# Performance work log

Hardware: AMD Instinct MI355X
Metric: run time of the kernel (lower is better)

The kernel has to match this reference:

```python
import jax, jax.numpy as jnp
import numpy as np

N_ATOMS, N_BONDS, B = 3072, 12288, 64
D, H, L = 256, 8, 4
AF, BF = 74, 12
HD = D // H
EPS = 1e-5


def layer_norm(x, g, b):
    m = jnp.mean(x, -1, keepdims=True)
    v = jnp.mean((x - m) ** 2, -1, keepdims=True)
    return (x - m) / jnp.sqrt(v + EPS) * g + b


def mha(x, in_w, in_b, out_w, out_b, mask=None):
    # torch nn.MultiheadAttention with packed in_proj, batch of 1 sequence
    n = x.shape[0]
    qkv = x @ in_w.T + in_b                      # [n, 3D]
    q, k, v = jnp.split(qkv, 3, axis=-1)
    q = q.reshape(n, H, HD)
    k = k.reshape(n, H, HD)
    v = v.reshape(n, H, HD)
    scores = jnp.einsum('qhd,khd->hqk', q, k) / jnp.asarray(np.sqrt(HD), x.dtype)
    if mask is not None:
        scores = jnp.where(mask[None], scores, jnp.asarray(-1e9, x.dtype))
    att = jax.nn.softmax(scores, axis=-1)
    out = jnp.einsum('hqk,khd->qhd', att, v).reshape(n, D)
    return out @ out_w.T + out_b


def setup_inputs() -> dict:
    key = jax.random.key(0)
    ks = jax.random.split(key, 12)
    s = 0.05
    return {
        'atom_features': jax.random.normal(ks[0], (N_ATOMS, AF), jnp.float32),
        'bond_features': jax.random.normal(ks[1], (N_BONDS, BF), jnp.float32),
        'edge_indices': jax.random.randint(ks[2], (2, N_BONDS), 0, N_ATOMS),
        'batch_idx': jnp.sort(jax.random.randint(ks[3], (N_ATOMS,), 0, B)),
        'atom_w': jax.random.normal(ks[4], (D, AF), jnp.float32) * s,
        'atom_b': jnp.zeros((D,), jnp.float32),
        'bond_w': jax.random.normal(ks[5], (D, BF), jnp.float32) * s,
        'bond_b': jnp.zeros((D,), jnp.float32),
        'conv_w': jax.random.normal(ks[6], (L, D, 2 * D), jnp.float32) * s,
        'conv_b': jnp.zeros((L, D), jnp.float32),
        'attn_in_w': jax.random.normal(ks[7], (L, 3 * D, D), jnp.float32) * s,
        'attn_in_b': jnp.zeros((L, 3 * D), jnp.float32),
        'attn_out_w': jax.random.normal(ks[8], (L, D, D), jnp.float32) * s,
        'attn_out_b': jnp.zeros((L, D), jnp.float32),
        'ln_g': jnp.ones((L, D), jnp.float32),
        'ln_b': jnp.zeros((L, D), jnp.float32),
        'gattn_in_w': jax.random.normal(ks[9], (3 * D, D), jnp.float32) * s,
        'gattn_in_b': jnp.zeros((3 * D,), jnp.float32),
        'gattn_out_w': jax.random.normal(ks[10], (D, D), jnp.float32) * s,
        'gattn_out_b': jnp.zeros((D,), jnp.float32),
        'gn_g': jnp.ones((D,), jnp.float32),
        'gn_b': jnp.zeros((D,), jnp.float32),
    }


def reference(atom_features, bond_features, edge_indices, batch_idx,
              atom_w, atom_b, bond_w, bond_b, conv_w, conv_b,
              attn_in_w, attn_in_b, attn_out_w, attn_out_b, ln_g, ln_b,
              gattn_in_w, gattn_in_b, gattn_out_w, gattn_out_b, gn_g, gn_b):
    atom_h = atom_features @ atom_w.T + atom_b       # [N, D]
    bond_h = bond_features @ bond_w.T + bond_b       # [E, D]
    src, tgt = edge_indices[0], edge_indices[1]
    for i in range(L):
        # gather -> concat -> linear -> relu -> scatter-add
        messages = jnp.concatenate([atom_h[src] + bond_h, atom_h[tgt]], axis=-1)
        messages = jax.nn.relu(messages @ conv_w[i].T + conv_b[i])
        aggregated = jnp.zeros_like(atom_h).at[tgt].add(messages)
        # self-attention over all atoms as a single sequence (as in source)
        attended = mha(atom_h, attn_in_w[i], attn_in_b[i], attn_out_w[i], attn_out_b[i])
        atom_h = layer_norm(atom_h + aggregated + attended, ln_g[i], ln_b[i])
    # per-graph pooled attention == full attention masked to same-graph pairs
    same_graph = batch_idx[:, None] == batch_idx[None, :]
    pooled = mha(atom_h, gattn_in_w, gattn_in_b, gattn_out_w, gattn_out_b, mask=same_graph)
    pooled = layer_norm(pooled, gn_g, gn_b)
    sums = jax.ops.segment_sum(pooled, batch_idx, num_segments=B)
    counts = jax.ops.segment_sum(jnp.ones((pooled.shape[0],), pooled.dtype), batch_idx, num_segments=B)
    return sums / jnp.maximum(counts, 1.0)[:, None]   # empty graphs -> zeros, as in source
```

## Files before the change

kernel.cpp:

```cpp
#include <hip/hip_runtime.h>
#include <hip/hip_bf16.h>
#include <math.h>

#define NATOMS 3072
#define NBONDS 12288
#define NGRAPH 64
#define DIM 256
#define NH 8
#define HDIM 32
#define NLAYER 4
#define AFD 74
#define BFD 12
#define LNEPS 1e-5f
#define HSZ (NATOMS * HDIM)

typedef __attribute__((ext_vector_type(8))) short bf16x8;
typedef __attribute__((ext_vector_type(4))) short s16x4;
typedef __attribute__((ext_vector_type(4))) float f32x4;

static __device__ __forceinline__ short f2bf(float x) {
  union { float f; unsigned u; } v; v.f = x;
  unsigned r = v.u + 0x7fff + ((v.u >> 16) & 1);
  return (short)(r >> 16);
}

static __device__ __forceinline__ float4 bf4tof4(s16x4 v) {
  union { unsigned u; float f; } x0, x1, x2, x3;
  x0.u = (unsigned)(unsigned short)v[0] << 16;
  x1.u = (unsigned)(unsigned short)v[1] << 16;
  x2.u = (unsigned)(unsigned short)v[2] << 16;
  x3.u = (unsigned)(unsigned short)v[3] << 16;
  return make_float4(x0.f, x1.f, x2.f, x3.f);
}

static __device__ __forceinline__ size_t afrag(int m, int c) {
  return ((size_t)(m >> 4) * 8 + (c >> 5)) * 512 + (m & 15) * 32 + (c & 31);
}

static __device__ __forceinline__ void gemm_core(
    const short* __restrict__ arow, const short* __restrict__ wch, f32x4* acc) {
  bf16x8 Xall[8];
  #pragma unroll
  for (int kc = 0; kc < 8; ++kc) Xall[kc] = *(const bf16x8*)(arow + kc * 512);
  bf16x8 Wb[2][4];
  #pragma unroll
  for (int sub = 0; sub < 4; ++sub) Wb[0][sub] = *(const bf16x8*)(wch + sub * 512);
  #pragma unroll
  for (int kc = 0; kc < 8; ++kc) {
    const int cur = kc & 1, nxt = cur ^ 1;
    if (kc < 7) {
      #pragma unroll
      for (int sub = 0; sub < 4; ++sub)
        Wb[nxt][sub] = *(const bf16x8*)(wch + (kc + 1) * 2048 + sub * 512);
    }
    __builtin_amdgcn_sched_barrier(0);
    #pragma unroll
    for (int sub = 0; sub < 4; ++sub)
      acc[sub] = __builtin_amdgcn_mfma_f32_16x16x32_bf16(Wb[cur][sub], Xall[kc], acc[sub], 0, 0, 0);
  }
}

#define CONVW_N8 65536
#define INW_N8   98304
#define OUTW_N8  32768
#define GINW_N8  24576
#define GOUTW_N8 8192
#define REPK_TOT (CONVW_N8 + INW_N8 + OUTW_N8 + GINW_N8 + GOUTW_N8)

static __device__ __forceinline__ void repack_one(
    const float* __restrict__ W, short* __restrict__ out, int kcShift, int o8) {
  const int g = o8 & 3, lq = (o8 >> 2) & 15, sub = (o8 >> 6) & 3;
  const int chunk = o8 >> 8;
  const int kc = chunk & ((1 << kcShift) - 1);
  const int nt = chunk >> kcShift;
  const int K = 32 << kcShift;
  const int n = nt * 64 + sub * 16 + lq;
  const int c = kc * 32 + g * 8;
  const float* src = W + (size_t)n * K + c;
  bf16x8 o;
  #pragma unroll
  for (int j = 0; j < 8; ++j) o[j] = f2bf(src[j]);
  ((bf16x8*)out)[o8] = o;
}

__global__ __launch_bounds__(256) void proj_hist_kernel(
    const float* __restrict__ afeat, const float* __restrict__ aw,
    const float* __restrict__ ab, float* __restrict__ atom_h,
    short* __restrict__ atom_hb, const float* __restrict__ bfeat,
    const float* __restrict__ bw, const float* __restrict__ bb,
    short* __restrict__ bond_hb, const int* __restrict__ tgt,
    int* __restrict__ counts) {
  const int idx = blockIdx.x, t = threadIdx.x;
  if (idx < NATOMS) {
    __shared__ float x[AFD];
    if (t < AFD) x[t] = afeat[idx * AFD + t];
    __syncthreads();
    float acc = ab[t];
    const float* wr = aw + t * AFD;
    for (int k = 0; k < AFD; ++k) acc = fmaf(wr[k], x[k], acc);
    atom_h[idx * DIM + t] = acc;
    atom_hb[afrag(idx, t)] = f2bf(acc);
  } else if (idx < NATOMS + NBONDS) {
    const int e = idx - NATOMS;
    __shared__ float xb[BFD];
    if (t < BFD) xb[t] = bfeat[e * BFD + t];
    __syncthreads();
    float acc = bb[t];
    const float* wr = bw + t * BFD;
    #pragma unroll
    for (int k = 0; k < BFD; ++k) acc = fmaf(wr[k], xb[k], acc);
    bond_hb[afrag(e, t)] = f2bf(acc);
  } else {
    const int e = (idx - NATOMS - NBONDS) * 256 + t;
    if (e < NBONDS) atomicAdd(&counts[tgt[e]], 1);
  }
}

__global__ __launch_bounds__(256) void scan_kernel(
    const int* __restrict__ counts, int* __restrict__ rowptr,
    int* __restrict__ cursor) {
  __shared__ int part[256];
  const int t = threadIdx.x;
  int loc[12], s = 0;
  #pragma unroll
  for (int j = 0; j < 12; ++j) { loc[j] = counts[t * 12 + j]; s += loc[j]; }
  part[t] = s;
  __syncthreads();
  for (int o = 1; o < 256; o <<= 1) {
    const int v = (t >= o) ? part[t - o] : 0;
    __syncthreads();
    part[t] += v;
    __syncthreads();
  }
  int running = part[t] - s;
  #pragma unroll
  for (int j = 0; j < 12; ++j) {
    rowptr[t * 12 + j] = running;
    cursor[t * 12 + j] = running;
    running += loc[j];
  }
  if (t == 255) rowptr[NATOMS] = running;
}

__global__ __launch_bounds__(256) void scatter_repack_kernel(
    const int* __restrict__ tgt, int* __restrict__ cursor, int* __restrict__ elist,
    const float* __restrict__ conv_w, const float* __restrict__ in_w,
    const float* __restrict__ out_w, const float* __restrict__ gin_w,
    const float* __restrict__ gout_w, short* __restrict__ conv_wb,
    short* __restrict__ in_wb, short* __restrict__ out_wb,
    short* __restrict__ gin_wb, short* __restrict__ gout_wb) {
  const int idx = blockIdx.x;
  if (idx < 48) {
    const int e = idx * 256 + threadIdx.x;
    if (e < NBONDS) {
      const int pos = atomicAdd(&cursor[tgt[e]], 1);
      elist[pos] = e;
    }
    return;
  }
  int o8 = (idx - 48) * 256 + threadIdx.x;
  if (o8 >= REPK_TOT) return;
  if (o8 < CONVW_N8) { repack_one(conv_w, conv_wb, 4, o8); return; }
  o8 -= CONVW_N8;
  if (o8 < INW_N8) { repack_one(in_w, in_wb, 3, o8); return; }
  o8 -= INW_N8;
  if (o8 < OUTW_N8) { repack_one(out_w, out_wb, 3, o8); return; }
  o8 -= OUTW_N8;
  if (o8 < GINW_N8) { repack_one(gin_w, gin_wb, 3, o8); return; }
  o8 -= GINW_N8;
  repack_one(gout_w, gout_wb, 3, o8);
}

__global__ __launch_bounds__(256) void layer_front_kernel(
    const short* __restrict__ atom_hb, const short* __restrict__ bond_hb,
    const short* __restrict__ cw, const short* __restrict__ inw,
    const float* __restrict__ inb, short* __restrict__ B1,
    short* __restrict__ G1, short* __restrict__ G2,
    short* __restrict__ Qb, short* __restrict__ Kff, short* __restrict__ Vtf,
    float qscale) {
  const int t = threadIdx.x;
  const int w = t >> 6, l = t & 63;
  const int lq = l & 15, g = l >> 4;
  const int lof = lq * 32 + g * 8;
  const int idx = blockIdx.x;
  f32x4 acc[4] = {{0.f,0.f,0.f,0.f},{0.f,0.f,0.f,0.f},{0.f,0.f,0.f,0.f},{0.f,0.f,0.f,0.f}};

  if (idx < 768) {
    const int by = idx / 384, bx = idx % 384;
    const int mrow = bx * 32 + (w & 1) * 16 + lq;
    const int nbase = by * 128 + (w >> 1) * 64;
    gemm_core(bond_hb + (size_t)(mrow >> 4) * 8 * 512 + lof,
              cw + (size_t)(nbase >> 6) * 16 * 2048 + lof, acc);
    #pragma unroll
    for (int sub = 0; sub < 4; ++sub) {
      const int n = nbase + sub * 16 + g * 4;
      s16x4 o;
      o[0] = f2bf(acc[sub][0]); o[1] = f2bf(acc[sub][1]);
      o[2] = f2bf(acc[sub][2]); o[3] = f2bf(acc[sub][3]);
      *(s16x4*)&B1[(size_t)mrow * DIM + n] = o;
    }
  } else if (idx < 1152) {
    const int i2 = idx - 768;
    const int bx = i2 % 96, by = i2 / 96;
    const int mrow = bx * 32 + (w & 1) * 16 + lq;
    const int nbase = by * 128 + (w >> 1) * 64;
    const int half = nbase >> 8, nl = nbase & 255;
    gemm_core(atom_hb + (size_t)(mrow >> 4) * 8 * 512 + lof,
              cw + ((size_t)(nl >> 6) * 16 + half * 8) * 2048 + lof, acc);
    short* C = half ? G2 : G1;
    #pragma unroll
    for (int sub = 0; sub < 4; ++sub) {
      const int n = nl + sub * 16 + g * 4;
      s16x4 o;
      o[0] = f2bf(acc[sub][0]); o[1] = f2bf(acc[sub][1]);
      o[2] = f2bf(acc[sub][2]); o[3] = f2bf(acc[sub][3]);
      *(s16x4*)&C[(size_t)mrow * DIM + n] = o;
    }
  } else {
    const int i3 = idx - 1152;
    const int bx = i3 % 96, by = i3 / 96;
    const int mrow = bx * 32 + (w & 1) * 16 + lq;
    const int nbase = by * 128 + (w >> 1) * 64;
    gemm_core(atom_hb + (size_t)(mrow >> 4) * 8 * 512 + lof,
              inw + (size_t)(nbase >> 6) * 8 * 2048 + lof, acc);
    const int key = mrow;
    #pragma unroll
    for (int sub = 0; sub < 4; ++sub) {
      const int n = nbase + sub * 16 + g * 4;
      const float4 b4 = *(const float4*)&inb[n];
      float4 v = make_float4(acc[sub][0] + b4.x, acc[sub][1] + b4.y,
                             acc[sub][2] + b4.z, acc[sub][3] + b4.w);
      if (n < 256) {
        s16x4 o;
        o[0] = f2bf(v.x * qscale); o[1] = f2bf(v.y * qscale);
        o[2] = f2bf(v.z * qscale); o[3] = f2bf(v.w * qscale);
        *(s16x4*)&Qb[afrag(mrow, n)] = o;
      } else if (n < 512) {
        const int d = n - 256, h = d >> 5, dd = d & 31;
        const size_t base = (size_t)h * HSZ + (size_t)(key >> 6) * 2048 +
                            (size_t)((key & 63) >> 4) * 512 +
                            ((dd >> 3) * 16 + (key & 15)) * 8 + (dd & 7);
        s16x4 o;
        o[0] = f2bf(v.x); o[1] = f2bf(v.y); o[2] = f2bf(v.z); o[3] = f2bf(v.w);
        *(s16x4*)&Kff[base] = o;
      } else {
        const int d = n - 512, h = d >> 5;
        const int kt = (key & 63) >> 5, gg = (key & 31) >> 3, j = key & 7;
        const int hh = (d & 31) >> 4;
        const size_t base = (size_t)h * HSZ + (size_t)(key >> 6) * 2048 +
                            (size_t)(kt * 2 + hh) * 512 + gg * 128 + j;
        Vtf[base + (size_t)((d + 0) & 15) * 8] = f2bf(v.x);
        Vtf[base + (size_t)((d + 1) & 15) * 8] = f2bf(v.y);
        Vtf[base + (size_t)((d + 2) & 15) * 8] = f2bf(v.z);
        Vtf[base + (size_t)((d + 3) & 15) * 8] = f2bf(v.w);
      }
    }
  }
}

static __device__ __forceinline__ void attn_body_full(
    int qtile, int h, const short* __restrict__ Qb,
    const short* __restrict__ Kff, const short* __restrict__ Vtf,
    short* __restrict__ outbf) {
  __shared__ short Ps[4][2][16 * 72];
  __shared__ float Comb[3][64][18];

  const int t = threadIdx.x;
  const int wid = t >> 6;
  const int l = t & 63;
  const int lq = l & 15;
  const int g = l >> 4;
  const int qt0 = qtile * 32;

  const bf16x8 Qf0 = *(const bf16x8*)(Qb + ((size_t)(qt0 >> 4) * 8 + h) * 512 + lq * 32 + g * 8);
  const bf16x8 Qf1 = *(const bf16x8*)(Qb + ((size_t)(qt0 >> 4) * 8 + 8 + h) * 512 + lq * 32 + g * 8);

  bf16x8 OnesF;
  #pragma unroll
  for (int j = 0; j < 8; ++j) OnesF[j] = (short)0x3F80;

  const short* kh = Kff + (size_t)h * HSZ + l * 8;
  const short* vh = Vtf + (size_t)h * HSZ + l * 8;

  f32x4 accO[2][2] = {{{0.f,0.f,0.f,0.f},{0.f,0.f,0.f,0.f}},
                      {{0.f,0.f,0.f,0.f},{0.f,0.f,0.f,0.f}}};
  f32x4 accL[2] = {{0.f,0.f,0.f,0.f},{0.f,0.f,0.f,0.f}};

  const int kbeg = wid * (NATOMS / 4);
  const int kend = kbeg + NATOMS / 4;

  bf16x8 Kf[2][4];
  bf16x8 Vf[2][4];

#define LOAD_TILE(buf, kc)                                                      \
  {                                                                             \
    const size_t tb = (size_t)((kc) >> 6) * 2048;                               \
    _Pragma("unroll")                                                           \
    for (int kk = 0; kk < 4; ++kk)                                              \
      Kf[buf][kk] = *(const bf16x8*)(kh + tb + kk * 512);                       \
    _Pragma("unroll")                                                           \
    for (int ff = 0; ff < 4; ++ff)                                              \
      Vf[buf][ff] = *(const bf16x8*)(vh + tb + ff * 512);                       \
  }

  LOAD_TILE(0, kbeg);

  for (int k0 = kbeg; k0 < kend; k0 += 128) {
    #pragma unroll
    for (int ph = 0; ph < 2; ++ph) {
      const int kcur = k0 + ph * 64;
      int kn = kcur + 64;
      if (kn >= kend) kn = kbeg;
      const int pb = ph ^ 1;
      LOAD_TILE(pb, kn);
      __builtin_amdgcn_sched_barrier(0);

      #pragma unroll
      for (int qt = 0; qt < 2; ++qt) {
        const bf16x8 Qf = qt ? Qf1 : Qf0;
        short* myPs = Ps[wid][qt];
        f32x4 s[4];
        #pragma unroll
        for (int kk = 0; kk < 4; ++kk)
          s[kk] = __builtin_amdgcn_mfma_f32_16x16x32_bf16(
              Kf[ph][kk], Qf, (f32x4){0.f, 0.f, 0.f, 0.f}, 0, 0, 0);
        #pragma unroll
        for (int kk = 0; kk < 4; ++kk) {
          const float p0 = __builtin_amdgcn_exp2f(s[kk][0]);
          const float p1 = __builtin_amdgcn_exp2f(s[kk][1]);
          const float p2 = __builtin_amdgcn_exp2f(s[kk][2]);
          const float p3 = __builtin_amdgcn_exp2f(s[kk][3]);
          unsigned u0, u1;
          asm("v_cvt_pk_bf16_f32 %0, %1, %2" : "=v"(u0) : "v"(p0), "v"(p1));
          asm("v_cvt_pk_bf16_f32 %0, %1, %2" : "=v"(u1) : "v"(p2), "v"(p3));
          *(uint2*)&myPs[lq * 72 + kk * 16 + g * 4] = make_uint2(u0, u1);
        }
      }

      #pragma unroll
      for (int qt = 0; qt < 2; ++qt) {
        #pragma unroll
        for (int kt = 0; kt < 2; ++kt) {
          const bf16x8 Pf = *(const bf16x8*)&Ps[wid][qt][lq * 72 + kt * 32 + g * 8];
          #pragma unroll
          for (int hh = 0; hh < 2; ++hh)
            accO[qt][hh] = __builtin_amdgcn_mfma_f32_16x16x32_bf16(
                Vf[ph][kt * 2 + hh], Pf, accO[qt][hh], 0, 0, 0);
          accL[qt] = __builtin_amdgcn_mfma_f32_16x16x32_bf16(OnesF, Pf, accL[qt], 0, 0, 0);
        }
      }
    }
  }
#undef LOAD_TILE

  if (wid > 0) {
    #pragma unroll
    for (int qt = 0; qt < 2; ++qt) {
      Comb[wid - 1][l][qt * 9] = accL[qt][0];
      #pragma unroll
      for (int hh = 0; hh < 2; ++hh)
        #pragma unroll
        for (int r = 0; r < 4; ++r)
          Comb[wid - 1][l][qt * 9 + 1 + hh * 4 + r] = accO[qt][hh][r];
    }
  }
  __syncthreads();
  if (wid == 0) {
    #pragma unroll
    for (int qt = 0; qt < 2; ++qt) {
      float tot = accL[qt][0];
      #pragma unroll
      for (int w2 = 0; w2 < 3; ++w2) {
        tot += Comb[w2][l][qt * 9];
        #pragma unroll
        for (int hh = 0; hh < 2; ++hh)
          #pragma unroll
          for (int r = 0; r < 4; ++r)
            accO[qt][hh][r] += Comb[w2][l][qt * 9 + 1 + hh * 4 + r];
      }
      const float inv = 1.f / tot;
      const int qrow = qt0 + qt * 16 + lq;
      #pragma unroll
      for (int hh = 0; hh < 2; ++hh) {
        s16x4 o;
        #pragma unroll
        for (int r = 0; r < 4; ++r) o[r] = f2bf(accO[qt][hh][r] * inv);
        *(s16x4*)&outbf[afrag(qrow, h * HDIM + hh * 16 + g * 4)] = o;
      }
    }
  }
}

static __device__ __forceinline__ void attn_body_masked(
    int qtile, int h, const short* __restrict__ Qb,
    const short* __restrict__ Kff, const short* __restrict__ Vtf,
    const int* __restrict__ bidx, short* __restrict__ outbf) {
  __shared__ short Ps[4][2][16 * 72];
  __shared__ float Comb[3][64][18];
  __shared__ int srange[2];

  const int t = threadIdx.x;
  const int wid = t >> 6;
  const int l = t & 63;
  const int lq = l & 15;
  const int g = l >> 4;
  const int qt0 = qtile * 32;

  if (t < 2) {
    const int target = (t == 0) ? bidx[qt0] : (bidx[qt0 + 31] + 1);
    int lo = 0, hi = NATOMS;
    while (lo < hi) {
      const int mid = (lo + hi) >> 1;
      if (bidx[mid] < target) lo = mid + 1; else hi = mid;
    }
    srange[t] = lo;
  }

  const bf16x8 Qf0 = *(const bf16x8*)(Qb + ((size_t)(qt0 >> 4) * 8 + h) * 512 + lq * 32 + g * 8);
  const bf16x8 Qf1 = *(const bf16x8*)(Qb + ((size_t)(qt0 >> 4) * 8 + 8 + h) * 512 + lq * 32 + g * 8);
  const int qg0 = bidx[qt0 + lq];
  const int qg1 = bidx[qt0 + 16 + lq];

  bf16x8 OnesF;
  #pragma unroll
  for (int j = 0; j < 8; ++j) OnesF[j] = (short)0x3F80;

  const short* kh = Kff + (size_t)h * HSZ + l * 8;
  const short* vh = Vtf + (size_t)h * HSZ + l * 8;

  f32x4 accO[2][2] = {{{0.f,0.f,0.f,0.f},{0.f,0.f,0.f,0.f}},
                      {{0.f,0.f,0.f,0.f},{0.f,0.f,0.f,0.f}}};
  f32x4 accL[2] = {{0.f,0.f,0.f,0.f},{0.f,0.f,0.f,0.f}};

  __syncthreads();
  const int t0 = srange[0] >> 6;
  const int t1 = (srange[1] + 63) >> 6;

  for (int tt = t0 + wid; tt < t1; tt += 4) {
    const int kc = tt * 64;
    const size_t tb = (size_t)tt * 2048;
    bf16x8 Kf[4], Vf[4];
    int4 KBv[4];
    #pragma unroll
    for (int kk = 0; kk < 4; ++kk) Kf[kk] = *(const bf16x8*)(kh + tb + kk * 512);
    #pragma unroll
    for (int ff = 0; ff < 4; ++ff) Vf[ff] = *(const bf16x8*)(vh + tb + ff * 512);
    #pragma unroll
    for (int kk = 0; kk < 4; ++kk) KBv[kk] = *(const int4*)(bidx + kc + kk * 16 + g * 4);

    #pragma unroll
    for (int qt = 0; qt < 2; ++qt) {
      const bf16x8 Qf = qt ? Qf1 : Qf0;
      const int qg = qt ? qg1 : qg0;
      short* myPs = Ps[wid][qt];
      f32x4 s[4];
      #pragma unroll
      for (int kk = 0; kk < 4; ++kk)
        s[kk] = __builtin_amdgcn_mfma_f32_16x16x32_bf16(
            Kf[kk], Qf, (f32x4){0.f, 0.f, 0.f, 0.f}, 0, 0, 0);
      #pragma unroll
      for (int kk = 0; kk < 4; ++kk) {
        float p0 = __builtin_amdgcn_exp2f(s[kk][0]);
        float p1 = __builtin_amdgcn_exp2f(s[kk][1]);
        float p2 = __builtin_amdgcn_exp2f(s[kk][2]);
        float p3 = __builtin_amdgcn_exp2f(s[kk][3]);
        const int4 kb = KBv[kk];
        p0 = (kb.x == qg) ? p0 : 0.f;
        p1 = (kb.y == qg) ? p1 : 0.f;
        p2 = (kb.z == qg) ? p2 : 0.f;
        p3 = (kb.w == qg) ? p3 : 0.f;
        unsigned u0, u1;
        asm("v_cvt_pk_bf16_f32 %0, %1, %2" : "=v"(u0) : "v"(p0), "v"(p1));
        asm("v_cvt_pk_bf16_f32 %0, %1, %2" : "=v"(u1) : "v"(p2), "v"(p3));
        *(uint2*)&myPs[lq * 72 + kk * 16 + g * 4] = make_uint2(u0, u1);
      }
    }

    #pragma unroll
    for (int qt = 0; qt < 2; ++qt) {
      #pragma unroll
      for (int kt = 0; kt < 2; ++kt) {
        const bf16x8 Pf = *(const bf16x8*)&Ps[wid][qt][lq * 72 + kt * 32 + g * 8];
        #pragma unroll
        for (int hh = 0; hh < 2; ++hh)
          accO[qt][hh] = __builtin_amdgcn_mfma_f32_16x16x32_bf16(
              Vf[kt * 2 + hh], Pf, accO[qt][hh], 0, 0, 0);
        accL[qt] = __builtin_amdgcn_mfma_f32_16x16x32_bf16(OnesF, Pf, accL[qt], 0, 0, 0);
      }
    }
  }

  if (wid > 0) {
    #pragma unroll
    for (int qt = 0; qt < 2; ++qt) {
      Comb[wid - 1][l][qt * 9] = accL[qt][0];
      #pragma unroll
      for (int hh = 0; hh < 2; ++hh)
        #pragma unroll
        for (int r = 0; r < 4; ++r)
          Comb[wid - 1][l][qt * 9 + 1 + hh * 4 + r] = accO[qt][hh][r];
    }
  }
  __syncthreads();
  if (wid == 0) {
    #pragma unroll
    for (int qt = 0; qt < 2; ++qt) {
      float tot = accL[qt][0];
      #pragma unroll
      for (int w2 = 0; w2 < 3; ++w2) {
        tot += Comb[w2][l][qt * 9];
        #pragma unroll
        for (int hh = 0; hh < 2; ++hh)
          #pragma unroll
          for (int r = 0; r < 4; ++r)
            accO[qt][hh][r] += Comb[w2][l][qt * 9 + 1 + hh * 4 + r];
      }
      const float inv = 1.f / tot;
      const int qrow = qt0 + qt * 16 + lq;
      #pragma unroll
      for (int hh = 0; hh < 2; ++hh) {
        s16x4 o;
        #pragma unroll
        for (int r = 0; r < 4; ++r) o[r] = f2bf(accO[qt][hh][r] * inv);
        *(s16x4*)&outbf[afrag(qrow, h * HDIM + hh * 16 + g * 4)] = o;
      }
    }
  }
}

static __device__ __forceinline__ void msg_body(
    int blk, const short* __restrict__ G1, const short* __restrict__ B1,
    const short* __restrict__ G2, const float* __restrict__ bias,
    const int* __restrict__ src, const int* __restrict__ rowptr,
    const int* __restrict__ elist, float* __restrict__ agg) {
  const int wv = threadIdx.x >> 6, lane = threadIdx.x & 63;
  const int t = blk * 4 + wv;
  const int c = lane * 4;
  const float4 bb = *(const float4*)&bias[c];
  const float4 g2 = bf4tof4(*(const s16x4*)&G2[(size_t)t * DIM + c]);
  const float gx = g2.x + bb.x, gy = g2.y + bb.y, gz = g2.z + bb.z, gw = g2.w + bb.w;
  float4 acc = make_float4(0.f, 0.f, 0.f, 0.f);
  const int beg = rowptr[t], end = rowptr[t + 1];
  for (int j = beg; j < end; ++j) {
    const int e = elist[j];
    const int s = src[e];
    const float4 g1 = bf4tof4(*(const s16x4*)&G1[(size_t)s * DIM + c]);
    const float4 b1 = bf4tof4(*(const s16x4*)&B1[(size_t)e * DIM + c]);
    acc.x += fmaxf(g1.x + b1.x + gx, 0.f);
    acc.y += fmaxf(g1.y + b1.y + gy, 0.f);
    acc.z += fmaxf(g1.z + b1.z + gz, 0.f);
    acc.w += fmaxf(g1.w + b1.w + gw, 0.f);
  }
  *(float4*)&agg[(size_t)t * DIM + c] = acc;
}

__global__ __launch_bounds__(256) void layer_mid_kernel(
    const short* __restrict__ Qb, const short* __restrict__ Kff,
    const short* __restrict__ Vtf, short* __restrict__ att_b,
    const short* __restrict__ G1, const short* __restrict__ B1,
    const short* __restrict__ G2, const float* __restrict__ bias,
    const int* __restrict__ src, const int* __restrict__ rowptr,
    const int* __restrict__ elist, float* __restrict__ agg) {
  const int idx = blockIdx.x;
  if (idx < 768) {
    attn_body_full(idx % 96, idx / 96, Qb, Kff, Vtf, att_b);
  } else {
    msg_body(idx - 768, G1, B1, G2, bias, src, rowptr, elist, agg);
  }
}

__global__ __launch_bounds__(256) void attn_masked_kernel(
    const short* __restrict__ Qb, const short* __restrict__ Kff,
    const short* __restrict__ Vtf, const int* __restrict__ bidx,
    short* __restrict__ outbf) {
  attn_body_masked(blockIdx.x, blockIdx.y, Qb, Kff, Vtf, bidx, outbf);
}

__global__ __launch_bounds__(256) void gemm_qkv_kernel(
    const short* __restrict__ A, const short* __restrict__ W,
    const float* __restrict__ bias, short* __restrict__ Qb,
    short* __restrict__ Kff, short* __restrict__ Vtf, float qscale) {
  const int t = threadIdx.x;
  const int w = t >> 6, l = t & 63;
  const int lq = l & 15, g = l >> 4;
  const int mrow = blockIdx.x * 32 + (w & 1) * 16 + lq;
  const int nbase = blockIdx.y * 128 + (w >> 1) * 64;
  const int lof = lq * 32 + g * 8;
  f32x4 acc[4] = {{0.f,0.f,0.f,0.f},{0.f,0.f,0.f,0.f},{0.f,0.f,0.f,0.f},{0.f,0.f,0.f,0.f}};
  gemm_core(A + (size_t)(mrow >> 4) * 8 * 512 + lof,
            W + (size_t)(nbase >> 6) * 8 * 2048 + lof, acc);
  const int key = mrow;
  #pragma unroll
  for (int sub = 0; sub < 4; ++sub) {
    const int n = nbase + sub * 16 + g * 4;
    const float4 b4 = *(const float4*)&bias[n];
    float4 v = make_float4(acc[sub][0] + b4.x, acc[sub][1] + b4.y,
                           acc[sub][2] + b4.z, acc[sub][3] + b4.w);
    if (n < 256) {
      s16x4 o;
      o[0] = f2bf(v.x * qscale); o[1] = f2bf(v.y * qscale);
      o[2] = f2bf(v.z * qscale); o[3] = f2bf(v.w * qscale);
      *(s16x4*)&Qb[afrag(mrow, n)] = o;
    } else if (n < 512) {
      const int d = n - 256, h = d >> 5, dd = d & 31;
      const size_t base = (size_t)h * HSZ + (size_t)(key >> 6) * 2048 +
                          (size_t)((key & 63) >> 4) * 512 +
                          ((dd >> 3) * 16 + (key & 15)) * 8 + (dd & 7);
      s16x4 o;
      o[0] = f2bf(v.x); o[1] = f2bf(v.y); o[2] = f2bf(v.z); o[3] = f2bf(v.w);
      *(s16x4*)&Kff[base] = o;
    } else {
      const int d = n - 512, h = d >> 5;
      const int kt = (key & 63) >> 5, gg = (key & 31) >> 3, j = key & 7;
      const int hh = (d & 31) >> 4;
      const size_t base = (size_t)h * HSZ + (size_t)(key >> 6) * 2048 +
                          (size_t)(kt * 2 + hh) * 512 + gg * 128 + j;
      Vtf[base + (size_t)((d + 0) & 15) * 8] = f2bf(v.x);
      Vtf[base + (size_t)((d + 1) & 15) * 8] = f2bf(v.y);
      Vtf[base + (size_t)((d + 2) & 15) * 8] = f2bf(v.z);
      Vtf[base + (size_t)((d + 3) & 15) * 8] = f2bf(v.w);
    }
  }
}

template <bool RESID>
__global__ __launch_bounds__(256) void outproj_ln_kernel(
    const short* __restrict__ A, const short* __restrict__ W,
    const float* __restrict__ bias, const float* __restrict__ r1,
    const float* __restrict__ r2, const float* __restrict__ g,
    const float* __restrict__ b, float* __restrict__ outf,
    short* __restrict__ outbf) {
  __shared__ float Red[4][2][16];
  const int t = threadIdx.x;
  const int w = t >> 6, l = t & 63;
  const int lq = l & 15, gg = l >> 4;
  const int mtile = blockIdx.x;
  const int mrow = mtile * 16 + lq;
  const int nbase = w * 64;
  const int lof = lq * 32 + gg * 8;
  f32x4 acc[4] = {{0.f,0.f,0.f,0.f},{0.f,0.f,0.f,0.f},{0.f,0.f,0.f,0.f},{0.f,0.f,0.f,0.f}};
  gemm_core(A + (size_t)mtile * 8 * 512 + lof,
            W + (size_t)(nbase >> 6) * 8 * 2048 + lof, acc);

  float y[4][4];
  float sp = 0.f, qp = 0.f;
  #pragma unroll
  for (int sub = 0; sub < 4; ++sub) {
    const int n = nbase + sub * 16 + gg * 4;
    const float4 b4 = *(const float4*)&bias[n];
    float4 v = make_float4(acc[sub][0] + b4.x, acc[sub][1] + b4.y,
                           acc[sub][2] + b4.z, acc[sub][3] + b4.w);
    if (RESID) {
      const size_t i2 = (size_t)mrow * DIM + n;
      const float4 a4 = *(const float4*)&r1[i2];
      const float4 c4 = *(const float4*)&r2[i2];
      v.x += a4.x + c4.x; v.y += a4.y + c4.y;
      v.z += a4.z + c4.z; v.w += a4.w + c4.w;
    }
    y[sub][0] = v.x; y[sub][1] = v.y; y[sub][2] = v.z; y[sub][3] = v.w;
    sp += (v.x + v.y) + (v.z + v.w);
    qp += (v.x * v.x + v.y * v.y) + (v.z * v.z + v.w * v.w);
  }
  sp += __shfl_xor(sp, 16); sp += __shfl_xor(sp, 32);
  qp += __shfl_xor(qp, 16); qp += __shfl_xor(qp, 32);
  if (l < 16) { Red[w][0][lq] = sp; Red[w][1][lq] = qp; }
  __syncthreads();
  const float s = Red[0][0][lq] + Red[1][0][lq] + Red[2][0][lq] + Red[3][0][lq];
  const float q = Red[0][1][lq] + Red[1][1][lq] + Red[2][1][lq] + Red[3][1][lq];
  const float mean = s * (1.f / 256.f);
  const float var = q * (1.f / 256.f) - mean * mean;
  const float rstd = rsqrtf(var + LNEPS);

  #pragma unroll
  for (int sub = 0; sub < 4; ++sub) {
    const int n = nbase + sub * 16 + gg * 4;
    const float4 g4 = *(const float4*)&g[n];
    const float4 b4 = *(const float4*)&b[n];
    float4 o;
    o.x = (y[sub][0] - mean) * rstd * g4.x + b4.x;
    o.y = (y[sub][1] - mean) * rstd * g4.y + b4.y;
    o.z = (y[sub][2] - mean) * rstd * g4.z + b4.z;
    o.w = (y[sub][3] - mean) * rstd * g4.w + b4.w;
    if (outf) *(float4*)&outf[(size_t)mrow * DIM + n] = o;
    if (outbf) {
      s16x4 ob;
      ob[0] = f2bf(o.x); ob[1] = f2bf(o.y); ob[2] = f2bf(o.z); ob[3] = f2bf(o.w);
      *(s16x4*)&outbf[afrag(mrow, n)] = ob;
    }
  }
}

__global__ __launch_bounds__(256) void pool_seg_kernel(
    const float* __restrict__ pooled, const int* __restrict__ bidx,
    float* __restrict__ out) {
  const int b = blockIdx.x, t = threadIdx.x;
  __shared__ int se[2];
  if (t < 2) {
    const int target = b + t;
    int lo = 0, hi = NATOMS;
    while (lo < hi) {
      const int mid = (lo + hi) >> 1;
      if (bidx[mid] < target) lo = mid + 1; else hi = mid;
    }
    se[t] = lo;
  }
  __syncthreads();
  const int beg = se[0], end = se[1];
  float acc = 0.f;
  for (int a = beg; a < end; ++a) acc += pooled[(size_t)a * DIM + t];
  out[(size_t)b * DIM + t] = acc / fmaxf((float)(end - beg), 1.f);
}

extern "C" void kernel_launch(void* const* d_in, const int* in_sizes, int n_in,
                              void* d_out, int out_size, void* d_ws, size_t ws_size,
                              hipStream_t stream) {
  const float* atom_features = (const float*)d_in[0];
  const float* bond_features = (const float*)d_in[1];
  const int* edge_indices = (const int*)d_in[2];
  const int* batch_idx = (const int*)d_in[3];
  const float* atom_w = (const float*)d_in[4];
  const float* atom_b = (const float*)d_in[5];
  const float* bond_w = (const float*)d_in[6];
  const float* bond_b = (const float*)d_in[7];
  const float* conv_w = (const float*)d_in[8];
  const float* conv_b = (const float*)d_in[9];
  const float* attn_in_w = (const float*)d_in[10];
  const float* attn_in_b = (const float*)d_in[11];
  const float* attn_out_w = (const float*)d_in[12];
  const float* attn_out_b = (const float*)d_in[13];
  const float* ln_g = (const float*)d_in[14];
  const float* ln_b = (const float*)d_in[15];
  const float* gattn_in_w = (const float*)d_in[16];
  const float* gattn_in_b = (const float*)d_in[17];
  const float* gattn_out_w = (const float*)d_in[18];
  const float* gattn_out_b = (const float*)d_in[19];
  const float* gn_g = (const float*)d_in[20];
  const float* gn_b = (const float*)d_in[21];

  const float QSCALE = 0.17677669529663687f * 1.4426950408889634f;

  char* wsb = (char*)d_ws;
  size_t off = 0;
  auto alloc_f = [&](size_t n) { float* p = (float*)(wsb + off); off += n * 4; return p; };
  auto alloc_s = [&](size_t n) { short* p = (short*)(wsb + off); off += n * 2; return p; };
  auto alloc_i = [&](size_t n) { int* p = (int*)(wsb + off); off += n * 4; return p; };

  float* atom_h = alloc_f((size_t)NATOMS * DIM);
  float* agg    = alloc_f((size_t)NATOMS * DIM);
  float* pooled = alloc_f((size_t)NATOMS * DIM);
  short* B1     = alloc_s((size_t)NBONDS * DIM);
  short* G1     = alloc_s((size_t)NATOMS * DIM);
  short* G2     = alloc_s((size_t)NATOMS * DIM);
  short* atom_hb = alloc_s((size_t)NATOMS * DIM);
  short* bond_hb = alloc_s((size_t)NBONDS * DIM);
  short* q_b     = alloc_s((size_t)NATOMS * DIM);
  short* kff_b   = alloc_s((size_t)NATOMS * DIM);
  short* vtf_b   = alloc_s((size_t)NATOMS * DIM);
  short* att_b   = alloc_s((size_t)NATOMS * DIM);
  short* conv_wb = alloc_s((size_t)NLAYER * DIM * 2 * DIM);
  short* in_wb   = alloc_s((size_t)NLAYER * 3 * DIM * DIM);
  short* out_wb  = alloc_s((size_t)NLAYER * DIM * DIM);
  short* gin_wb  = alloc_s((size_t)3 * DIM * DIM);
  short* gout_wb = alloc_s((size_t)DIM * DIM);
  int* counts = alloc_i(NATOMS);
  int* rowptr = alloc_i(NATOMS + 1);
  int* cursor = alloc_i(NATOMS);
  int* elist  = alloc_i(NBONDS);
  if (ws_size < off) return;

  const int* src = edge_indices;
  const int* tgt = edge_indices + NBONDS;

  hipMemsetAsync(counts, 0, NATOMS * sizeof(int), stream);
  proj_hist_kernel<<<NATOMS + NBONDS + NBONDS / 256, 256, 0, stream>>>(
      atom_features, atom_w, atom_b, atom_h, atom_hb,
      bond_features, bond_w, bond_b, bond_hb, tgt, counts);
  scan_kernel<<<1, 256, 0, stream>>>(counts, rowptr, cursor);
  scatter_repack_kernel<<<48 + REPK_TOT / 256, 256, 0, stream>>>(
      tgt, cursor, elist, conv_w, attn_in_w, attn_out_w, gattn_in_w, gattn_out_w,
      conv_wb, in_wb, out_wb, gin_wb, gout_wb);

  for (int i = 0; i < NLAYER; ++i) {
    layer_front_kernel<<<1728, 256, 0, stream>>>(
        atom_hb, bond_hb, conv_wb + (size_t)i * DIM * 2 * DIM,
        in_wb + (size_t)i * 3 * DIM * DIM, attn_in_b + (size_t)i * 3 * DIM,
        B1, G1, G2, q_b, kff_b, vtf_b, QSCALE);
    layer_mid_kernel<<<1536, 256, 0, stream>>>(
        q_b, kff_b, vtf_b, att_b, G1, B1, G2, conv_b + (size_t)i * DIM,
        src, rowptr, elist, agg);
    outproj_ln_kernel<true><<<NATOMS / 16, 256, 0, stream>>>(
        att_b, out_wb + (size_t)i * DIM * DIM, attn_out_b + (size_t)i * DIM,
        atom_h, agg, ln_g + (size_t)i * DIM, ln_b + (size_t)i * DIM,
        atom_h, atom_hb);
  }

  gemm_qkv_kernel<<<dim3(96, 6), 256, 0, stream>>>(
      atom_hb, gin_wb, gattn_in_b, q_b, kff_b, vtf_b, QSCALE);
  attn_masked_kernel<<<dim3(96, 8), 256, 0, stream>>>(
      q_b, kff_b, vtf_b, batch_idx, att_b);
  outproj_ln_kernel<false><<<NATOMS / 16, 256, 0, stream>>>(
      att_b, gout_wb, gattn_out_b, nullptr, nullptr, gn_g, gn_b,
      pooled, nullptr);

  pool_seg_kernel<<<NGRAPH, 256, 0, stream>>>(pooled, batch_idx, (float*)d_out);
}
```

Before: 297.3 us.

## Hoist bond GEMM for all layers and widen attention query tile to 64

The bond-feature times conv-weight product does not depend on the layer's atom state, so it is moved out of the per-layer front kernel into one launch that precomputes B1 for all four layers. Each layer's front kernel then only handles the atom GEMMs, which shortens the critical path. The full-attention body now processes 64 queries per block instead of 32, halving how often K/V tiles are reloaded per query and halving the attention block count. Shared memory for P and the combine buffer is aliased, and a sync is added before reuse. The cost is extra workspace (four B1 buffers), more registers per attention wave, and fewer attention blocks to fill the GPU.

```diff
diff --git a/kernel.cpp b/kernel.cpp
--- a/kernel.cpp
+++ b/kernel.cpp
@@ -171,10 +171,36 @@
   repack_one(gout_w, gout_wb, 3, o8);
 }
 
+__global__ __launch_bounds__(256) void bond_all_kernel(
+    const short* __restrict__ bond_hb, const short* __restrict__ conv_wb,
+    short* __restrict__ B1all) {
+  const int t = threadIdx.x;
+  const int w = t >> 6, l = t & 63;
+  const int lq = l & 15, g = l >> 4;
+  const int lof = lq * 32 + g * 8;
+  const int layer = blockIdx.x / 768;
+  const int r = blockIdx.x % 768;
+  const int by = r / 384, bx = r % 384;
+  const int mrow = bx * 32 + (w & 1) * 16 + lq;
+  const int nbase = by * 128 + (w >> 1) * 64;
+  const short* cw = conv_wb + (size_t)layer * DIM * 2 * DIM;
+  short* B1 = B1all + (size_t)layer * NBONDS * DIM;
+  f32x4 acc[4] = {{0.f,0.f,0.f,0.f},{0.f,0.f,0.f,0.f},{0.f,0.f,0.f,0.f},{0.f,0.f,0.f,0.f}};
+  gemm_core(bond_hb + (size_t)(mrow >> 4) * 8 * 512 + lof,
+            cw + (size_t)(nbase >> 6) * 16 * 2048 + lof, acc);
+  #pragma unroll
+  for (int sub = 0; sub < 4; ++sub) {
+    const int n = nbase + sub * 16 + g * 4;
+    s16x4 o;
+    o[0] = f2bf(acc[sub][0]); o[1] = f2bf(acc[sub][1]);
+    o[2] = f2bf(acc[sub][2]); o[3] = f2bf(acc[sub][3]);
+    *(s16x4*)&B1[(size_t)mrow * DIM + n] = o;
+  }
+}
+
 __global__ __launch_bounds__(256) void layer_front_kernel(
-    const short* __restrict__ atom_hb, const short* __restrict__ bond_hb,
-    const short* __restrict__ cw, const short* __restrict__ inw,
-    const float* __restrict__ inb, short* __restrict__ B1,
+    const short* __restrict__ atom_hb, const short* __restrict__ cw,
+    const short* __restrict__ inw, const float* __restrict__ inb,
     short* __restrict__ G1, short* __restrict__ G2,
     short* __restrict__ Qb, short* __restrict__ Kff, short* __restrict__ Vtf,
     float qscale) {
@@ -185,23 +211,8 @@
   const int idx = blockIdx.x;
   f32x4 acc[4] = {{0.f,0.f,0.f,0.f},{0.f,0.f,0.f,0.f},{0.f,0.f,0.f,0.f},{0.f,0.f,0.f,0.f}};
 
-  if (idx < 768) {
-    const int by = idx / 384, bx = idx % 384;
-    const int mrow = bx * 32 + (w & 1) * 16 + lq;
-    const int nbase = by * 128 + (w >> 1) * 64;
-    gemm_core(bond_hb + (size_t)(mrow >> 4) * 8 * 512 + lof,
-              cw + (size_t)(nbase >> 6) * 16 * 2048 + lof, acc);
-    #pragma unroll
-    for (int sub = 0; sub < 4; ++sub) {
-      const int n = nbase + sub * 16 + g * 4;
-      s16x4 o;
-      o[0] = f2bf(acc[sub][0]); o[1] = f2bf(acc[sub][1]);
-      o[2] = f2bf(acc[sub][2]); o[3] = f2bf(acc[sub][3]);
-      *(s16x4*)&B1[(size_t)mrow * DIM + n] = o;
-    }
-  } else if (idx < 1152) {
-    const int i2 = idx - 768;
-    const int bx = i2 % 96, by = i2 / 96;
+  if (idx < 384) {
+    const int bx = idx % 96, by = idx / 96;
     const int mrow = bx * 32 + (w & 1) * 16 + lq;
     const int nbase = by * 128 + (w >> 1) * 64;
     const int half = nbase >> 8, nl = nbase & 255;
@@ -217,7 +228,7 @@
       *(s16x4*)&C[(size_t)mrow * DIM + n] = o;
     }
   } else {
-    const int i3 = idx - 1152;
+    const int i3 = idx - 384;
     const int bx = i3 % 96, by = i3 / 96;
     const int mrow = bx * 32 + (w & 1) * 16 + lq;
     const int nbase = by * 128 + (w >> 1) * 64;
@@ -258,22 +269,26 @@
   }
 }
 
-static __device__ __forceinline__ void attn_body_full(
+static __device__ __forceinline__ void attn_body_full4(
     int qtile, int h, const short* __restrict__ Qb,
     const short* __restrict__ Kff, const short* __restrict__ Vtf,
     short* __restrict__ outbf) {
-  __shared__ short Ps[4][2][16 * 72];
-  __shared__ float Comb[3][64][18];
+  __shared__ __align__(16) char smem[27648];
+  short (*Ps)[2][1152] = (short (*)[2][1152])smem;
+  float (*Comb)[64][36] = (float (*)[64][36])smem;
 
   const int t = threadIdx.x;
   const int wid = t >> 6;
   const int l = t & 63;
   const int lq = l & 15;
   const int g = l >> 4;
-  const int qt0 = qtile * 32;
-
-  const bf16x8 Qf0 = *(const bf16x8*)(Qb + ((size_t)(qt0 >> 4) * 8 + h) * 512 + lq * 32 + g * 8);
-  const bf16x8 Qf1 = *(const bf16x8*)(Qb + ((size_t)(qt0 >> 4) * 8 + 8 + h) * 512 + lq * 32 + g * 8);
+  const int qt0 = qtile * 64;
+  const int mt0 = qt0 >> 4;
+
+  bf16x8 Qf[4];
+  #pragma unroll
+  for (int qt = 0; qt < 4; ++qt)
+    Qf[qt] = *(const bf16x8*)(Qb + ((size_t)(mt0 + qt) * 8 + h) * 512 + lq * 32 + g * 8);
 
   bf16x8 OnesF;
   #pragma unroll
@@ -282,9 +297,14 @@
   const short* kh = Kff + (size_t)h * HSZ + l * 8;
   const short* vh = Vtf + (size_t)h * HSZ + l * 8;
 
-  f32x4 accO[2][2] = {{{0.f,0.f,0.f,0.f},{0.f,0.f,0.f,0.f}},
-                      {{0.f,0.f,0.f,0.f},{0.f,0.f,0.f,0.f}}};
-  f32x4 accL[2] = {{0.f,0.f,0.f,0.f},{0.f,0.f,0.f,0.f}};
+  f32x4 accO[4][2];
+  f32x4 accL[4];
+  #pragma unroll
+  for (int qt = 0; qt < 4; ++qt) {
+    accO[qt][0] = (f32x4){0.f, 0.f, 0.f, 0.f};
+    accO[qt][1] = (f32x4){0.f, 0.f, 0.f, 0.f};
+    accL[qt] = (f32x4){0.f, 0.f, 0.f, 0.f};
+  }
 
   const int kbeg = wid * (NATOMS / 4);
   const int kend = kbeg + NATOMS / 4;
@@ -316,46 +336,50 @@
       __builtin_amdgcn_sched_barrier(0);
 
       #pragma unroll
-      for (int qt = 0; qt < 2; ++qt) {
-        const bf16x8 Qf = qt ? Qf1 : Qf0;
-        short* myPs = Ps[wid][qt];
-        f32x4 s[4];
+      for (int qph = 0; qph < 2; ++qph) {
         #pragma unroll
-        for (int kk = 0; kk < 4; ++kk)
-          s[kk] = __builtin_amdgcn_mfma_f32_16x16x32_bf16(
-              Kf[ph][kk], Qf, (f32x4){0.f, 0.f, 0.f, 0.f}, 0, 0, 0);
+        for (int q2 = 0; q2 < 2; ++q2) {
+          const int qt = qph * 2 + q2;
+          short* myPs = Ps[wid][q2];
+          f32x4 s[4];
+          #pragma unroll
+          for (int kk = 0; kk < 4; ++kk)
+            s[kk] = __builtin_amdgcn_mfma_f32_16x16x32_bf16(
+                Kf[ph][kk], Qf[qt], (f32x4){0.f, 0.f, 0.f, 0.f}, 0, 0, 0);
+          #pragma unroll
+          for (int kk = 0; kk < 4; ++kk) {
+            const float p0 = __builtin_amdgcn_exp2f(s[kk][0]);
+            const float p1 = __builtin_amdgcn_exp2f(s[kk][1]);
+            const float p2 = __builtin_amdgcn_exp2f(s[kk][2]);
+            const float p3 = __builtin_amdgcn_exp2f(s[kk][3]);
+            unsigned u0, u1;
+            asm("v_cvt_pk_bf16_f32 %0, %1, %2" : "=v"(u0) : "v"(p0), "v"(p1));
+            asm("v_cvt_pk_bf16_f32 %0, %1, %2" : "=v"(u1) : "v"(p2), "v"(p3));
+            *(uint2*)&myPs[lq * 72 + kk * 16 + g * 4] = make_uint2(u0, u1);
+          }
+        }
         #pragma unroll
-        for (int kk = 0; kk < 4; ++kk) {
-          const float p0 = __builtin_amdgcn_exp2f(s[kk][0]);
-          const float p1 = __builtin_amdgcn_exp2f(s[kk][1]);
-          const float p2 = __builtin_amdgcn_exp2f(s[kk][2]);
-          const float p3 = __builtin_amdgcn_exp2f(s[kk][3]);
-          unsigned u0, u1;
-          asm("v_cvt_pk_bf16_f32 %0, %1, %2" : "=v"(u0) : "v"(p0), "v"(p1));
-          asm("v_cvt_pk_bf16_f32 %0, %1, %2" : "=v"(u1) : "v"(p2), "v"(p3));
-          *(uint2*)&myPs[lq * 72 + kk * 16 + g * 4] = make_uint2(u0, u1);
+        for (int q2 = 0; q2 < 2; ++q2) {
+          const int qt = qph * 2 + q2;
+          #pragma unroll
+          for (int kt = 0; kt < 2; ++kt) {
+            const bf16x8 Pf = *(const bf16x8*)&Ps[wid][q2][lq * 72 + kt * 32 + g * 8];
+            #pragma unroll
+            for (int hh = 0; hh < 2; ++hh)
+              accO[qt][hh] = __builtin_amdgcn_mfma_f32_16x16x32_bf16(
+                  Vf[ph][kt * 2 + hh], Pf, accO[qt][hh], 0, 0, 0);
+            accL[qt] = __builtin_amdgcn_mfma_f32_16x16x32_bf16(OnesF, Pf, accL[qt], 0, 0, 0);
+          }
         }
       }
-
-      #pragma unroll
-      for (int qt = 0; qt < 2; ++qt) {
-        #pragma unroll
-        for (int kt = 0; kt < 2; ++kt) {
-          const bf16x8 Pf = *(const bf16x8*)&Ps[wid][qt][lq * 72 + kt * 32 + g * 8];
-          #pragma unroll
-          for (int hh = 0; hh < 2; ++hh)
-            accO[qt][hh] = __builtin_amdgcn_mfma_f32_16x16x32_bf16(
-                Vf[ph][kt * 2 + hh], Pf, accO[qt][hh], 0, 0, 0);
-          accL[qt] = __builtin_amdgcn_mfma_f32_16x16x32_bf16(OnesF, Pf, accL[qt], 0, 0, 0);
-        }
-      }
     }
   }
 #undef LOAD_TILE
 
+  __syncthreads();
   if (wid > 0) {
     #pragma unroll
-    for (int qt = 0; qt < 2; ++qt) {
+    for (int qt = 0; qt < 4; ++qt) {
       Comb[wid - 1][l][qt * 9] = accL[qt][0];
       #pragma unroll
       for (int hh = 0; hh < 2; ++hh)
@@ -367,7 +391,7 @@
   __syncthreads();
   if (wid == 0) {
     #pragma unroll
-    for (int qt = 0; qt < 2; ++qt) {
+    for (int qt = 0; qt < 4; ++qt) {
       float tot = accL[qt][0];
       #pragma unroll
       for (int w2 = 0; w2 < 3; ++w2) {
@@ -562,10 +586,10 @@
     const int* __restrict__ src, const int* __restrict__ rowptr,
     const int* __restrict__ elist, float* __restrict__ agg) {
   const int idx = blockIdx.x;
-  if (idx < 768) {
-    attn_body_full(idx % 96, idx / 96, Qb, Kff, Vtf, att_b);
+  if (idx < 384) {
+    attn_body_full4(idx % 48, idx / 48, Qb, Kff, Vtf, att_b);
   } else {
-    msg_body(idx - 768, G1, B1, G2, bias, src, rowptr, elist, agg);
+    msg_body(idx - 384, G1, B1, G2, bias, src, rowptr, elist, agg);
   }
 }
 
@@ -748,7 +772,7 @@
   float* atom_h = alloc_f((size_t)NATOMS * DIM);
   float* agg    = alloc_f((size_t)NATOMS * DIM);
   float* pooled = alloc_f((size_t)NATOMS * DIM);
-  short* B1     = alloc_s((size_t)NBONDS * DIM);
+  short* B1all  = alloc_s((size_t)NLAYER * NBONDS * DIM);
   short* G1     = alloc_s((size_t)NATOMS * DIM);
   short* G2     = alloc_s((size_t)NATOMS * DIM);
   short* atom_hb = alloc_s((size_t)NATOMS * DIM);
@@ -779,15 +803,16 @@
   scatter_repack_kernel<<<48 + REPK_TOT / 256, 256, 0, stream>>>(
       tgt, cursor, elist, conv_w, attn_in_w, attn_out_w, gattn_in_w, gattn_out_w,
       conv_wb, in_wb, out_wb, gin_wb, gout_wb);
+  bond_all_kernel<<<NLAYER * 768, 256, 0, stream>>>(bond_hb, conv_wb, B1all);
 
   for (int i = 0; i < NLAYER; ++i) {
-    layer_front_kernel<<<1728, 256, 0, stream>>>(
-        atom_hb, bond_hb, conv_wb + (size_t)i * DIM * 2 * DIM,
+    layer_front_kernel<<<960, 256, 0, stream>>>(
+        atom_hb, conv_wb + (size_t)i * DIM * 2 * DIM,
         in_wb + (size_t)i * 3 * DIM * DIM, attn_in_b + (size_t)i * 3 * DIM,
-        B1, G1, G2, q_b, kff_b, vtf_b, QSCALE);
-    layer_mid_kernel<<<1536, 256, 0, stream>>>(
-        q_b, kff_b, vtf_b, att_b, G1, B1, G2, conv_b + (size_t)i * DIM,
-        src, rowptr, elist, agg);
+        G1, G2, q_b, kff_b, vtf_b, QSCALE);
+    layer_mid_kernel<<<1152, 256, 0, stream>>>(
+        q_b, kff_b, vtf_b, att_b, G1, B1all + (size_t)i * NBONDS * DIM, G2,
+        conv_b + (size_t)i * DIM, src, rowptr, elist, agg);
     outproj_ln_kernel<true><<<NATOMS / 16, 256, 0, stream>>>(
         att_b, out_wb + (size_t)i * DIM * DIM, attn_out_b + (size_t)i * DIM,
         atom_h, agg, ln_g + (size_t)i * DIM, ln_b + (size_t)i * DIM,
```

Result: slower. 315.8 us (+6.2%).

## Hoist bond-feature conv GEMM for all layers into one upfront kernel

Applied to the files above, without the earlier changes.

The bond_h times conv_w GEMM does not depend on the evolving atom state, so it now runs once for all four layers in a single large launch before the layer loop, writing into a per-layer B1 buffer. Each layer's front kernel shrinks to the atom-side GEMMs only. The aim is better occupancy from one big launch and a shorter per-layer critical path. The cost is four times more workspace for B1 (about 25 MB of bf16) and more memory traffic that may no longer stay in cache.

```diff
diff --git a/kernel.cpp b/kernel.cpp
--- a/kernel.cpp
+++ b/kernel.cpp
@@ -171,10 +171,36 @@
   repack_one(gout_w, gout_wb, 3, o8);
 }
 
+__global__ __launch_bounds__(256) void bond_all_kernel(
+    const short* __restrict__ bond_hb, const short* __restrict__ conv_wb,
+    short* __restrict__ B1all) {
+  const int t = threadIdx.x;
+  const int w = t >> 6, l = t & 63;
+  const int lq = l & 15, g = l >> 4;
+  const int lof = lq * 32 + g * 8;
+  const int layer = blockIdx.x / 768;
+  const int r = blockIdx.x % 768;
+  const int by = r / 384, bx = r % 384;
+  const int mrow = bx * 32 + (w & 1) * 16 + lq;
+  const int nbase = by * 128 + (w >> 1) * 64;
+  const short* cw = conv_wb + (size_t)layer * DIM * 2 * DIM;
+  short* B1 = B1all + (size_t)layer * NBONDS * DIM;
+  f32x4 acc[4] = {{0.f,0.f,0.f,0.f},{0.f,0.f,0.f,0.f},{0.f,0.f,0.f,0.f},{0.f,0.f,0.f,0.f}};
+  gemm_core(bond_hb + (size_t)(mrow >> 4) * 8 * 512 + lof,
+            cw + (size_t)(nbase >> 6) * 16 * 2048 + lof, acc);
+  #pragma unroll
+  for (int sub = 0; sub < 4; ++sub) {
+    const int n = nbase + sub * 16 + g * 4;
+    s16x4 o;
+    o[0] = f2bf(acc[sub][0]); o[1] = f2bf(acc[sub][1]);
+    o[2] = f2bf(acc[sub][2]); o[3] = f2bf(acc[sub][3]);
+    *(s16x4*)&B1[(size_t)mrow * DIM + n] = o;
+  }
+}
+
 __global__ __launch_bounds__(256) void layer_front_kernel(
-    const short* __restrict__ atom_hb, const short* __restrict__ bond_hb,
-    const short* __restrict__ cw, const short* __restrict__ inw,
-    const float* __restrict__ inb, short* __restrict__ B1,
+    const short* __restrict__ atom_hb, const short* __restrict__ cw,
+    const short* __restrict__ inw, const float* __restrict__ inb,
     short* __restrict__ G1, short* __restrict__ G2,
     short* __restrict__ Qb, short* __restrict__ Kff, short* __restrict__ Vtf,
     float qscale) {
@@ -185,23 +211,8 @@
   const int idx = blockIdx.x;
   f32x4 acc[4] = {{0.f,0.f,0.f,0.f},{0.f,0.f,0.f,0.f},{0.f,0.f,0.f,0.f},{0.f,0.f,0.f,0.f}};
 
-  if (idx < 768) {
-    const int by = idx / 384, bx = idx % 384;
-    const int mrow = bx * 32 + (w & 1) * 16 + lq;
-    const int nbase = by * 128 + (w >> 1) * 64;
-    gemm_core(bond_hb + (size_t)(mrow >> 4) * 8 * 512 + lof,
-              cw + (size_t)(nbase >> 6) * 16 * 2048 + lof, acc);
-    #pragma unroll
-    for (int sub = 0; sub < 4; ++sub) {
-      const int n = nbase + sub * 16 + g * 4;
-      s16x4 o;
-      o[0] = f2bf(acc[sub][0]); o[1] = f2bf(acc[sub][1]);
-      o[2] = f2bf(acc[sub][2]); o[3] = f2bf(acc[sub][3]);
-      *(s16x4*)&B1[(size_t)mrow * DIM + n] = o;
-    }
-  } else if (idx < 1152) {
-    const int i2 = idx - 768;
-    const int bx = i2 % 96, by = i2 / 96;
+  if (idx < 384) {
+    const int bx = idx % 96, by = idx / 96;
     const int mrow = bx * 32 + (w & 1) * 16 + lq;
     const int nbase = by * 128 + (w >> 1) * 64;
     const int half = nbase >> 8, nl = nbase & 255;
@@ -217,7 +228,7 @@
       *(s16x4*)&C[(size_t)mrow * DIM + n] = o;
     }
   } else {
-    const int i3 = idx - 1152;
+    const int i3 = idx - 384;
     const int bx = i3 % 96, by = i3 / 96;
     const int mrow = bx * 32 + (w & 1) * 16 + lq;
     const int nbase = by * 128 + (w >> 1) * 64;
@@ -748,7 +759,7 @@
   float* atom_h = alloc_f((size_t)NATOMS * DIM);
   float* agg    = alloc_f((size_t)NATOMS * DIM);
   float* pooled = alloc_f((size_t)NATOMS * DIM);
-  short* B1     = alloc_s((size_t)NBONDS * DIM);
+  short* B1all  = alloc_s((size_t)NLAYER * NBONDS * DIM);
   short* G1     = alloc_s((size_t)NATOMS * DIM);
   short* G2     = alloc_s((size_t)NATOMS * DIM);
   short* atom_hb = alloc_s((size_t)NATOMS * DIM);
@@ -779,15 +790,16 @@
   scatter_repack_kernel<<<48 + REPK_TOT / 256, 256, 0, stream>>>(
       tgt, cursor, elist, conv_w, attn_in_w, attn_out_w, gattn_in_w, gattn_out_w,
       conv_wb, in_wb, out_wb, gin_wb, gout_wb);
+  bond_all_kernel<<<NLAYER * 768, 256, 0, stream>>>(bond_hb, conv_wb, B1all);
 
   for (int i = 0; i < NLAYER; ++i) {
-    layer_front_kernel<<<1728, 256, 0, stream>>>(
-        atom_hb, bond_hb, conv_wb + (size_t)i * DIM * 2 * DIM,
+    layer_front_kernel<<<960, 256, 0, stream>>>(
+        atom_hb, conv_wb + (size_t)i * DIM * 2 * DIM,
         in_wb + (size_t)i * 3 * DIM * DIM, attn_in_b + (size_t)i * 3 * DIM,
-        B1, G1, G2, q_b, kff_b, vtf_b, QSCALE);
+        G1, G2, q_b, kff_b, vtf_b, QSCALE);
     layer_mid_kernel<<<1536, 256, 0, stream>>>(
-        q_b, kff_b, vtf_b, att_b, G1, B1, G2, conv_b + (size_t)i * DIM,
-        src, rowptr, elist, agg);
+        q_b, kff_b, vtf_b, att_b, G1, B1all + (size_t)i * NBONDS * DIM, G2,
+        conv_b + (size_t)i * DIM, src, rowptr, elist, agg);
     outproj_ln_kernel<true><<<NATOMS / 16, 256, 0, stream>>>(
         att_b, out_wb + (size_t)i * DIM * DIM, attn_out_b + (size_t)i * DIM,
         atom_h, agg, ln_g + (size_t)i * DIM, ln_b + (size_t)i * DIM,
```

After: 299.9 us. About the same (+0.9%).
